# Kernel optimization log

Hardware: AMD Instinct MI355X
Metric: run time of the kernel (lower is better)

## Reference

```python
import jax, jax.numpy as jnp
import numpy as np

N = 50000          # num nodes
E = 800000         # num edges (before self loops)
IN_C = 128
HID = 256          # heads * head_dim
HEADS = 4
HEAD_DIM = HID // HEADS
OUT_C = 64
NEG_SLOPE = 0.2    # PyG GATConv default leaky_relu slope
BN_EPS = 1e-5


def _gat_conv(x, src, dst, W, att_src, att_dst, bias, concat):
    """PyG-style GATConv (with self loops already appended to src/dst).
    x: [N, in_c]; W: [in_c, H*C]; att_src/att_dst: [H, C]; bias: [H*C] or [C]."""
    H, C = att_src.shape
    h = (x @ W).reshape(-1, H, C)                               # [N, H, C]
    a_src = jnp.einsum('nhc,hc->nh', h, att_src)                # [N, H]
    a_dst = jnp.einsum('nhc,hc->nh', h, att_dst)                # [N, H]
    e = jax.nn.leaky_relu(a_src[src] + a_dst[dst], NEG_SLOPE)   # [Et, H]
    # segment softmax over destination nodes (numerically stable)
    m = jax.ops.segment_max(e, dst, num_segments=N)             # [N, H]
    m = jnp.where(jnp.isfinite(m), m, 0.0)
    ex = jnp.exp(e - m[dst])
    denom = jax.ops.segment_sum(ex, dst, num_segments=N)        # [N, H]
    alpha = ex / (denom[dst] + 1e-16)                           # [Et, H]
    msg = alpha[:, :, None] * h[src]                            # [Et, H, C]
    out = jax.ops.segment_sum(msg, dst, num_segments=N)         # [N, H, C]
    out = out.reshape(N, H * C) if concat else out.mean(axis=1)
    return out + bias


def _bn_eval(x, gamma, beta, mean, var):
    return (x - mean) * jax.lax.rsqrt(var + BN_EPS) * gamma + beta


def setup_inputs() -> dict:
    key = jax.random.key(0)
    ks = jax.random.split(key, 16)
    x = jax.random.normal(ks[0], (N, IN_C), dtype=jnp.float32)
    edge_index = jax.random.randint(ks[1], (2, E), 0, N, dtype=jnp.int64)

    def lin(k, fan_in, fan_out):
        s = (1.0 / np.sqrt(fan_in)).astype(np.float32)
        return jax.random.normal(k, (fan_in, fan_out), dtype=jnp.float32) * s

    def att(k, h, c):
        return jax.random.normal(k, (h, c), dtype=jnp.float32) * 0.1

    return {
        'x': x, 'edge_index': edge_index,
        'W0': lin(ks[2], IN_C, HID), 'as0': att(ks[3], HEADS, HEAD_DIM), 'ad0': att(ks[4], HEADS, HEAD_DIM), 'b0': jnp.zeros((HID,), jnp.float32),
        'bn0_g': jnp.ones((HID,), jnp.float32), 'bn0_b': jnp.zeros((HID,), jnp.float32), 'bn0_m': jnp.zeros((HID,), jnp.float32), 'bn0_v': jnp.ones((HID,), jnp.float32),
        'W1': lin(ks[5], HID, HID), 'as1': att(ks[6], HEADS, HEAD_DIM), 'ad1': att(ks[7], HEADS, HEAD_DIM), 'b1': jnp.zeros((HID,), jnp.float32),
        'bn1_g': jnp.ones((HID,), jnp.float32), 'bn1_b': jnp.zeros((HID,), jnp.float32), 'bn1_m': jnp.zeros((HID,), jnp.float32), 'bn1_v': jnp.ones((HID,), jnp.float32),
        'W2': lin(ks[8], HID, OUT_C), 'as2': att(ks[9], 1, OUT_C), 'ad2': att(ks[10], 1, OUT_C), 'b2': jnp.zeros((OUT_C,), jnp.float32),
    }


def reference(x, edge_index, W0, as0, ad0, b0, bn0_g, bn0_b, bn0_m, bn0_v,
              W1, as1, ad1, b1, bn1_g, bn1_b, bn1_m, bn1_v,
              W2, as2, ad2, b2):
    loop = jnp.arange(N, dtype=edge_index.dtype)
    src = jnp.concatenate([edge_index[0], loop])   # PyG add_self_loops=True
    dst = jnp.concatenate([edge_index[1], loop])

    h = _gat_conv(x, src, dst, W0, as0, ad0, b0, concat=True)
    h = jax.nn.elu(_bn_eval(h, bn0_g, bn0_b, bn0_m, bn0_v))   # dropout: eval -> identity
    h = _gat_conv(h, src, dst, W1, as1, ad1, b1, concat=True)
    h = jax.nn.elu(_bn_eval(h, bn1_g, bn1_b, bn1_m, bn1_v))
    out = _gat_conv(h, src, dst, W2, as2, ad2, b2, concat=False)  # heads=1, mean
    return out
```

## Files before the change

### kernel.cpp

```cpp
#include <hip/hip_runtime.h>

#define NN   50000
#define EE   800000
#define ET   850000
#define INC  128
#define HID  256
#define OUTC 64
#define NEG  0.2f
#define BNEPS 1e-5f

typedef __bf16 bf16x8 __attribute__((ext_vector_type(8)));
typedef float  f32x4  __attribute__((ext_vector_type(4)));

static __device__ __forceinline__ float b2f(unsigned short u) {
    return __uint_as_float(((unsigned)u) << 16);
}
static __device__ __forceinline__ float blo(unsigned u) {
    return __uint_as_float(u << 16);
}
static __device__ __forceinline__ float bhi(unsigned u) {
    return __uint_as_float(u & 0xFFFF0000u);
}
static __device__ __forceinline__ unsigned short f2b(float f) {
    unsigned u = __float_as_uint(f);
    unsigned r = u + 0x7FFFu + ((u >> 16) & 1u);
    return (unsigned short)(r >> 16);
}
static __device__ __forceinline__ float leaky(float x) {
    return x > 0.f ? x : NEG * x;
}
static __device__ __forceinline__ float ew(float e) {
    return __expf(fminf(e, 80.f));
}

__global__ void k_init(const int* __restrict__ ei, const unsigned* __restrict__ xw,
                       int* __restrict__ cnt, int* __restrict__ flagW, int* __restrict__ flagB,
                       int nbZ) {
    __shared__ int cs[4];
    int b = blockIdx.x, t = threadIdx.x;
    if (b < nbZ) {
        int i = b * 256 + t;
        if (i < NN) cnt[i] = 0;
    } else if (b == nbZ) {
        int c = 0;
        for (int k = 0; k < 16; k++) {
            int i = t + 256 * k;
            if (ei[2 * i + 1] != 0) c = 1;
        }
        for (int o = 1; o < 64; o <<= 1) c |= __shfl_xor(c, o);
        if ((t & 63) == 0) cs[t >> 6] = c;
        __syncthreads();
        if (t == 0) *flagW = cs[0] | cs[1] | cs[2] | cs[3];
    } else {
        int c = 0;
        for (int i = t; i < 4096; i += 256) {
            unsigned v = (xw[i] >> 8) & 0x7F;
            if (v >= 50 && v <= 67) c++;
        }
        for (int o = 1; o < 64; o <<= 1) c += __shfl_xor(c, o);
        if ((t & 63) == 0) cs[t >> 6] = c;
        __syncthreads();
        if (t == 0) *flagB = (cs[0] + cs[1] + cs[2] + cs[3] > 2048) ? 1 : 0;
    }
}

__global__ void k_prep(const void* as0, const void* ad0, const void* b0, const void* g0,
                       const void* be0, const void* m0, const void* v0,
                       const void* as1, const void* ad1, const void* b1, const void* g1,
                       const void* be1, const void* m1, const void* v1,
                       const void* as2, const void* ad2, const void* b2,
                       const void* W0, const void* W1, const void* W2,
                       unsigned short* __restrict__ WT0, unsigned short* __restrict__ WT1,
                       unsigned short* __restrict__ WT2,
                       const void* __restrict__ x, unsigned short* __restrict__ xb,
                       float* __restrict__ pp, const int* __restrict__ flagB) {
    int b = blockIdx.x, t = threadIdx.x;
    bool bf = (*flagB != 0);
    auto cv = [&](const void* s, int i) -> float {
        return bf ? b2f(((const unsigned short*)s)[i]) : ((const float*)s)[i];
    };
    if (b < 14) {
        float v;
        switch (b) {
            case 0:  v = cv(as0, t); break;
            case 1:  v = cv(ad0, t); break;
            case 2:  v = cv(b0, t);  break;
            case 3:  v = cv(g0, t);  break;
            case 4:  v = cv(be0, t); break;
            case 5:  v = cv(m0, t);  break;
            case 6:  v = cv(v0, t);  break;
            case 7:  v = cv(as1, t); break;
            case 8:  v = cv(ad1, t); break;
            case 9:  v = cv(b1, t);  break;
            case 10: v = cv(g1, t);  break;
            case 11: v = cv(be1, t); break;
            case 12: v = cv(m1, t);  break;
            default: v = cv(v1, t);  break;
        }
        pp[b * 256 + t] = v;
    } else if (b == 14) {
        if (t < 192) {
            int arr = t >> 6, j = t & 63;
            float v = (arr == 0) ? cv(as2, j) : (arr == 1) ? cv(ad2, j) : cv(b2, j);
            pp[14 * 256 + arr * 64 + j] = v;
        }
    } else if (b < 15 + 128) {
        int i = (b - 15) * 256 + t;
        int k = i >> 8, n = i & 255;
        WT0[n * INC + k] = bf ? ((const unsigned short*)W0)[i] : f2b(((const float*)W0)[i]);
    } else if (b < 15 + 128 + 256) {
        int i = (b - 143) * 256 + t;
        int k = i >> 8, n = i & 255;
        WT1[n * HID + k] = bf ? ((const unsigned short*)W1)[i] : f2b(((const float*)W1)[i]);
    } else if (b < 15 + 128 + 256 + 64) {
        int i = (b - 399) * 256 + t;
        int k = i >> 6, n = i & 63;
        WT2[n * HID + k] = bf ? ((const unsigned short*)W2)[i] : f2b(((const float*)W2)[i]);
    } else {
        if (bf) return;
        int i = (b - 463) * 256 + t;
        if (i < NN * INC)
            xb[i] = f2b(((const float*)x)[i]);
    }
}

__global__ void k_hist(const int* __restrict__ ei, const int* __restrict__ flagW,
                       int* __restrict__ cnt) {
    int i = blockIdx.x * 256 + threadIdx.x;
    if (i >= ET) return;
    bool w32 = (*flagW != 0);
    int d = (i < EE) ? (w32 ? ei[EE + i] : ei[2 * (EE + i)]) : (i - EE);
    atomicAdd(&cnt[d], 1);
}

static __device__ __forceinline__ int block_scan_incl(int v, int t, int* ws) {
    int lane = t & 63, w = t >> 6;
    int x = v;
    for (int o = 1; o < 64; o <<= 1) {
        int y = __shfl_up(x, o);
        if (lane >= o) x += y;
    }
    if (lane == 63) ws[w] = x;
    __syncthreads();
    if (t == 0) {
        int s = 0;
        for (int k = 0; k < 4; k++) { int tmp = ws[k]; ws[k] = s; s += tmp; }
    }
    __syncthreads();
    return x + ws[w];
}

__global__ void k_scan_a(const int* __restrict__ cnt, int* __restrict__ rowptr, int* __restrict__ bsum) {
    __shared__ int ws[4];
    int t = threadIdx.x, b = blockIdx.x;
    int i = b * 256 + t;
    int v = (i < NN) ? cnt[i] : 0;
    int incl = block_scan_incl(v, t, ws);
    if (i < NN) rowptr[i] = incl - v;
    if (t == 255) bsum[b] = incl;
}

__global__ void k_scan_b(int* __restrict__ bsum, int nb) {
    __shared__ int ws[4];
    int t = threadIdx.x;
    int v = (t < nb) ? bsum[t] : 0;
    int incl = block_scan_incl(v, t, ws);
    if (t < nb) bsum[t] = incl - v;
}

__global__ void k_scan_c(int* __restrict__ rowptr, const int* __restrict__ bsum, int* __restrict__ cursor) {
    int t = threadIdx.x, b = blockIdx.x;
    int i = b * 256 + t;
    if (i < NN) {
        int r = rowptr[i] + bsum[b];
        rowptr[i] = r;
        cursor[i] = r;
    }
    if (i == 0) rowptr[NN] = ET;
}

__global__ void k_scatter(const int* __restrict__ ei, const int* __restrict__ flagW,
                          int* __restrict__ cursor, int* __restrict__ esrc) {
    int i = blockIdx.x * 256 + threadIdx.x;
    if (i >= ET) return;
    bool w32 = (*flagW != 0);
    int s, d;
    if (i < EE) {
        if (w32) { s = ei[i];     d = ei[EE + i]; }
        else     { s = ei[2 * i]; d = ei[2 * (EE + i)]; }
    } else {
        s = d = i - EE;
    }
    int p = atomicAdd(&cursor[d], 1);
    esrc[p] = s;
}

template<int NC, int NH>
__global__ __launch_bounds__(256) void k_gemm(const unsigned short* __restrict__ Amain,
                                              const void* __restrict__ Aalt,
                                              const int* __restrict__ flagB,
                                              const unsigned short* __restrict__ WT,
                                              unsigned short* __restrict__ H,
                                              float* __restrict__ asrc, float* __restrict__ adst,
                                              const float* __restrict__ asv, const float* __restrict__ adv,
                                              int M, int K) {
    __shared__ __align__(16) unsigned short As[128 * 40];
    __shared__ __align__(16) unsigned short Bs[64 * 40];
    const unsigned short* A = (*flagB) ? (const unsigned short*)Aalt : Amain;
    int t = threadIdx.x;
    int bm = blockIdx.x, bn = blockIdx.y;
    int lane = t & 63, wave = t >> 6;
    int m16 = lane & 15, quad = lane >> 4;

    f32x4 acc[2][4];
    for (int a = 0; a < 2; a++) for (int b = 0; b < 4; b++) acc[a][b] = (f32x4){0.f, 0.f, 0.f, 0.f};

    int arow = t >> 1, ahalf = t & 1;
    int brow = t >> 2, bq = t & 3;
    long gArow = (long)bm * 128 + arow;

    for (int k0 = 0; k0 < K; k0 += 32) {
        uint4 av0 = {0u, 0u, 0u, 0u}, av1 = {0u, 0u, 0u, 0u};
        if (gArow < M) {
            const unsigned short* ap = A + gArow * (size_t)K + k0 + ahalf * 16;
            av0 = *(const uint4*)(ap);
            av1 = *(const uint4*)(ap + 8);
        }
        uint4 bv = *(const uint4*)(WT + ((size_t)bn * 64 + brow) * K + k0 + bq * 8);
        *(uint4*)&As[arow * 40 + ahalf * 16]     = av0;
        *(uint4*)&As[arow * 40 + ahalf * 16 + 8] = av1;
        *(uint4*)&Bs[brow * 40 + bq * 8]         = bv;
        __syncthreads();
        int wrow = wave * 32;
        bf16x8 af[2], bf[4];
        for (int mt = 0; mt < 2; mt++)
            af[mt] = *(const bf16x8*)&As[(wrow + mt * 16 + m16) * 40 + quad * 8];
        for (int nt = 0; nt < 4; nt++)
            bf[nt] = *(const bf16x8*)&Bs[(nt * 16 + m16) * 40 + quad * 8];
        for (int mt = 0; mt < 2; mt++)
            for (int nt = 0; nt < 4; nt++)
                acc[mt][nt] = __builtin_amdgcn_mfma_f32_16x16x32_bf16(af[mt], bf[nt], acc[mt][nt], 0, 0, 0);
        __syncthreads();
    }

    float asc[4], adc[4];
    for (int nt = 0; nt < 4; nt++) {
        int col = bn * 64 + nt * 16 + m16;
        asc[nt] = asv[col];
        adc[nt] = adv[col];
    }
    for (int mt = 0; mt < 2; mt++) {
        int gR0 = bm * 128 + wave * 32 + mt * 16 + quad * 4;
        for (int r = 0; r < 4; r++) {
            int gR = gR0 + r;
            float ps = 0.f, pd = 0.f;
            for (int nt = 0; nt < 4; nt++) {
                float v = acc[mt][nt][r];
                ps += v * asc[nt];
                pd += v * adc[nt];
            }
            for (int o = 1; o < 16; o <<= 1) { ps += __shfl_xor(ps, o); pd += __shfl_xor(pd, o); }
            if (m16 == 0 && gR < M) {
                asrc[(size_t)gR * NH + bn] = ps;
                adst[(size_t)gR * NH + bn] = pd;
            }
            if (gR < M) {
                for (int nt = 0; nt < 4; nt++) {
                    int gC = bn * 64 + nt * 16 + m16;
                    H[(size_t)gR * NC + gC] = f2b(acc[mt][nt][r]);
                }
            }
        }
    }
}

__global__ void k_agg4(const unsigned short* __restrict__ h,
                       const float* __restrict__ asrc, const float* __restrict__ adst,
                       const int* __restrict__ rowptr, const int* __restrict__ esrc,
                       const float* __restrict__ bias,
                       const float* __restrict__ bng, const float* __restrict__ bnb,
                       const float* __restrict__ bnm, const float* __restrict__ bnv,
                       unsigned short* __restrict__ act) {
    int t = threadIdx.x;
    int wave = t >> 6, lane = t & 63;
    int nodeA = blockIdx.x * 8 + wave * 2;
    if (nodeA >= NN) return;
    int nodeB = nodeA + 1;
    bool hasB = (nodeB < NN);

    int hd = lane >> 4, li = lane & 15;
    int wsel = lane & 48;
    const size_t lc = (size_t)lane * 4;

    int e0A = rowptr[nodeA];
    int e1A = rowptr[nodeA + 1];
    int degA = e1A - e0A;
    int e0B = 0, degB = 0;
    if (hasB) { e0B = e1A; degB = rowptr[nodeB + 1] - e1A; }
    float adhA = adst[(size_t)nodeA * 4 + hd];
    float adhB = hasB ? adst[(size_t)nodeB * 4 + hd] : 0.f;

    float waccA = 0.f, waccB = 0.f;
    float aA0 = 0.f, aA1 = 0.f, aA2 = 0.f, aA3 = 0.f;
    float aB0 = 0.f, aB1 = 0.f, aB2 = 0.f, aB3 = 0.f;

    int nA = min(16, degA), nB = min(16, degB);
    int sA = 0, sB = 0; float eA = 0.f, eB = 0.f;
    if (li < nA) { sA = esrc[e0A + li]; eA = asrc[(size_t)sA * 4 + hd]; }
    if (li < nB) { sB = esrc[e0B + li]; eB = asrc[(size_t)sB * 4 + hd]; }

    int degM = max(degA, degB);
    for (int c = 0; c < degM; c += 16) {
        float wA = (li < nA) ? ew(leaky(eA + adhA)) : 0.f;
        float wB = (li < nB) ? ew(leaky(eB + adhB)) : 0.f;
        waccA += wA; waccB += wB;
        int nA2 = min(16, degA - (c + 16));
        int nB2 = min(16, degB - (c + 16));
        int sA2 = 0, sB2 = 0; float eA2 = 0.f, eB2 = 0.f;
        if (li < nA2) { sA2 = esrc[e0A + c + 16 + li]; eA2 = asrc[(size_t)sA2 * 4 + hd]; }
        if (li < nB2) { sB2 = esrc[e0B + c + 16 + li]; eB2 = asrc[(size_t)sB2 * 4 + hd]; }
        #pragma unroll
        for (int g = 0; g < 4; g++) {
            int j = g * 4;
            bool doA = j < nA, doB = j < nB;
            int s0A = 0, s1A = 0, s2A = 0, s3A = 0;
            float w0A = 0.f, w1A = 0.f, w2A = 0.f, w3A = 0.f;
            ushort4 hA0 = {0, 0, 0, 0}, hA1 = {0, 0, 0, 0}, hA2 = {0, 0, 0, 0}, hA3 = {0, 0, 0, 0};
            int s0B = 0, s1B = 0, s2B = 0, s3B = 0;
            float w0B = 0.f, w1B = 0.f, w2B = 0.f, w3B = 0.f;
            ushort4 hB0 = {0, 0, 0, 0}, hB1 = {0, 0, 0, 0}, hB2 = {0, 0, 0, 0}, hB3 = {0, 0, 0, 0};
            if (doA) {
                s0A = __shfl(sA, j);     s1A = __shfl(sA, j + 1);
                s2A = __shfl(sA, j + 2); s3A = __shfl(sA, j + 3);
                w0A = __shfl(wA, wsel + j);     w1A = __shfl(wA, wsel + j + 1);
                w2A = __shfl(wA, wsel + j + 2); w3A = __shfl(wA, wsel + j + 3);
                hA0 = *(const ushort4*)(h + (size_t)s0A * HID + lc);
                hA1 = *(const ushort4*)(h + (size_t)s1A * HID + lc);
                hA2 = *(const ushort4*)(h + (size_t)s2A * HID + lc);
                hA3 = *(const ushort4*)(h + (size_t)s3A * HID + lc);
            }
            if (doB) {
                s0B = __shfl(sB, j);     s1B = __shfl(sB, j + 1);
                s2B = __shfl(sB, j + 2); s3B = __shfl(sB, j + 3);
                w0B = __shfl(wB, wsel + j);     w1B = __shfl(wB, wsel + j + 1);
                w2B = __shfl(wB, wsel + j + 2); w3B = __shfl(wB, wsel + j + 3);
                hB0 = *(const ushort4*)(h + (size_t)s0B * HID + lc);
                hB1 = *(const ushort4*)(h + (size_t)s1B * HID + lc);
                hB2 = *(const ushort4*)(h + (size_t)s2B * HID + lc);
                hB3 = *(const ushort4*)(h + (size_t)s3B * HID + lc);
            }
            if (doA) {
                aA0 += w0A * b2f(hA0.x) + w1A * b2f(hA1.x) + w2A * b2f(hA2.x) + w3A * b2f(hA3.x);
                aA1 += w0A * b2f(hA0.y) + w1A * b2f(hA1.y) + w2A * b2f(hA2.y) + w3A * b2f(hA3.y);
                aA2 += w0A * b2f(hA0.z) + w1A * b2f(hA1.z) + w2A * b2f(hA2.z) + w3A * b2f(hA3.z);
                aA3 += w0A * b2f(hA0.w) + w1A * b2f(hA1.w) + w2A * b2f(hA2.w) + w3A * b2f(hA3.w);
            }
            if (doB) {
                aB0 += w0B * b2f(hB0.x) + w1B * b2f(hB1.x) + w2B * b2f(hB2.x) + w3B * b2f(hB3.x);
                aB1 += w0B * b2f(hB0.y) + w1B * b2f(hB1.y) + w2B * b2f(hB2.y) + w3B * b2f(hB3.y);
                aB2 += w0B * b2f(hB0.z) + w1B * b2f(hB1.z) + w2B * b2f(hB2.z) + w3B * b2f(hB3.z);
                aB3 += w0B * b2f(hB0.w) + w1B * b2f(hB1.w) + w2B * b2f(hB2.w) + w3B * b2f(hB3.w);
            }
        }
        sA = sA2; eA = eA2; nA = nA2;
        sB = sB2; eB = eB2; nB = nB2;
    }
    waccA += __shfl_xor(waccA, 1); waccA += __shfl_xor(waccA, 2);
    waccA += __shfl_xor(waccA, 4); waccA += __shfl_xor(waccA, 8);
    waccB += __shfl_xor(waccB, 1); waccB += __shfl_xor(waccB, 2);
    waccB += __shfl_xor(waccB, 4); waccB += __shfl_xor(waccB, 8);
    float invA = 1.f / (waccA + 1e-16f);
    float invB = 1.f / (waccB + 1e-16f);

    int c0 = lane * 4;
    float4 bi = *(const float4*)(bias + c0);
    float4 bm_ = *(const float4*)(bnm + c0);
    float4 bv_ = *(const float4*)(bnv + c0);
    float4 bg_ = *(const float4*)(bng + c0);
    float4 bb_ = *(const float4*)(bnb + c0);
    float sc[4], sh[4];
    {
        const float* bvp = (const float*)&bv_;
        const float* bgp = (const float*)&bg_;
        const float* bmp = (const float*)&bm_;
        const float* bbp = (const float*)&bb_;
        const float* bip = (const float*)&bi;
        #pragma unroll
        for (int jj = 0; jj < 4; jj++) {
            float s_ = rsqrtf(bvp[jj] + BNEPS) * bgp[jj];
            sc[jj] = s_;
            sh[jj] = bbp[jj] + (bip[jj] - bmp[jj]) * s_;
        }
    }
    {
        float o[4] = {aA0 * invA, aA1 * invA, aA2 * invA, aA3 * invA};
        unsigned short res[4];
        #pragma unroll
        for (int jj = 0; jj < 4; jj++) {
            float val = o[jj] * sc[jj] + sh[jj];
            val = val > 0.f ? val : expm1f(val);
            res[jj] = f2b(val);
        }
        *(ushort4*)(act + (size_t)nodeA * HID + c0) = *(ushort4*)res;
    }
    if (hasB) {
        float o[4] = {aB0 * invB, aB1 * invB, aB2 * invB, aB3 * invB};
        unsigned short res[4];
        #pragma unroll
        for (int jj = 0; jj < 4; jj++) {
            float val = o[jj] * sc[jj] + sh[jj];
            val = val > 0.f ? val : expm1f(val);
            res[jj] = f2b(val);
        }
        *(ushort4*)(act + (size_t)nodeB * HID + c0) = *(ushort4*)res;
    }
}

__global__ __launch_bounds__(256, 4) void k_agg1(const unsigned short* __restrict__ h,
                       const float* __restrict__ asrc, const float* __restrict__ adst,
                       const int* __restrict__ rowptr, const int* __restrict__ esrc,
                       const float* __restrict__ bias,
                       void* __restrict__ outp, const int* __restrict__ flagB) {
    int t = threadIdx.x;
    int wave = t >> 6, lane = t & 63;
    int node = blockIdx.x * 4 + wave;
    if (node >= NN) return;
    int e0 = rowptr[node], deg = rowptr[node + 1] - e0;
    float ad = adst[node];
    int q = lane >> 4, laneQ = lane & 15;
    const size_t lc4 = (size_t)laneQ * 4;

    float den = 0.f;
    float a0 = 0.f, a1 = 0.f, a2 = 0.f, a3 = 0.f;

    int n = min(64, deg);
    int s = 0; float e = 0.f;
    if (lane < n) {
        s = esrc[e0 + lane];
        e = asrc[s];
    }

    for (int c = 0; c < deg; c += 64) {
        float w = (lane < n) ? ew(leaky(e + ad)) : 0.f;
        int n2 = min(64, deg - (c + 64));
        int sN = 0; float eN = 0.f;
        if (lane < n2) {
            sN = esrc[e0 + c + 64 + lane];
            eN = asrc[sN];
        }
        den += w;
        int ng = (n + 15) >> 4;
        #pragma unroll
        for (int g = 0; g < 4; g++) {
            if (g >= ng) break;
            int eb = g * 16 + q;
            int sA = __shfl(s, eb),      sB = __shfl(s, eb + 4);
            int sC = __shfl(s, eb + 8),  sD = __shfl(s, eb + 12);
            float wA = __shfl(w, eb),     wB = __shfl(w, eb + 4);
            float wC = __shfl(w, eb + 8), wD = __shfl(w, eb + 12);
            uint2 vA = *(const uint2*)(h + (size_t)sA * OUTC + lc4);
            uint2 vB = *(const uint2*)(h + (size_t)sB * OUTC + lc4);
            uint2 vC = *(const uint2*)(h + (size_t)sC * OUTC + lc4);
            uint2 vD = *(const uint2*)(h + (size_t)sD * OUTC + lc4);
            a0 += wA * blo(vA.x) + wB * blo(vB.x) + wC * blo(vC.x) + wD * blo(vD.x);
            a1 += wA * bhi(vA.x) + wB * bhi(vB.x) + wC * bhi(vC.x) + wD * bhi(vD.x);
            a2 += wA * blo(vA.y) + wB * blo(vB.y) + wC * blo(vC.y) + wD * blo(vD.y);
            a3 += wA * bhi(vA.y) + wB * bhi(vB.y) + wC * bhi(vC.y) + wD * bhi(vD.y);
        }
        s = sN; e = eN; n = n2;
    }
    for (int o = 1; o < 64; o <<= 1) den += __shfl_xor(den, o);
    a0 += __shfl_xor(a0, 16); a1 += __shfl_xor(a1, 16);
    a2 += __shfl_xor(a2, 16); a3 += __shfl_xor(a3, 16);
    a0 += __shfl_xor(a0, 32); a1 += __shfl_xor(a1, 32);
    a2 += __shfl_xor(a2, 32); a3 += __shfl_xor(a3, 32);
    float inv = 1.f / (den + 1e-16f);
    if (q == 0) {
        int c0 = laneQ * 4;
        float v0 = a0 * inv + bias[c0];
        float v1 = a1 * inv + bias[c0 + 1];
        float v2 = a2 * inv + bias[c0 + 2];
        float v3 = a3 * inv + bias[c0 + 3];
        if (*flagB) {
            unsigned r0 = (unsigned)f2b(v0) | ((unsigned)f2b(v1) << 16);
            unsigned r1 = (unsigned)f2b(v2) | ((unsigned)f2b(v3) << 16);
            uint2 rv = {r0, r1};
            *(uint2*)((unsigned short*)outp + (size_t)node * OUTC + c0) = rv;
        } else {
            float4 rv = {v0, v1, v2, v3};
            *(float4*)((float*)outp + (size_t)node * OUTC + c0) = rv;
        }
    }
}

extern "C" void kernel_launch(void* const* d_in, const int* in_sizes, int n_in,
                              void* d_out, int out_size, void* d_ws, size_t ws_size,
                              hipStream_t stream) {
    const void* x  = d_in[0];
    const int*  ei = (const int*)d_in[1];
    const void* W0 = d_in[2];
    const void* W1 = d_in[10];
    const void* W2 = d_in[18];

    char* ws = (char*)d_ws;
    size_t off = 0;
    auto alloc = [&](size_t n) { void* p = ws + off; off += (n + 255) & ~(size_t)255; return p; };

    unsigned short* xb  = (unsigned short*)alloc((size_t)NN * INC * 2);
    unsigned short* h   = (unsigned short*)alloc((size_t)NN * HID * 2);
    unsigned short* act = (unsigned short*)alloc((size_t)NN * HID * 2);
    unsigned short* WT0 = (unsigned short*)alloc((size_t)HID * INC * 2);
    unsigned short* WT1 = (unsigned short*)alloc((size_t)HID * HID * 2);
    unsigned short* WT2 = (unsigned short*)alloc((size_t)OUTC * HID * 2);
    float*          pp  = (float*)alloc((size_t)(14 * 256 + 3 * 64) * 4);
    float*  asrc   = (float*)alloc((size_t)NN * 4 * 4);
    float*  adst   = (float*)alloc((size_t)NN * 4 * 4);
    int*    cnt    = (int*)alloc((size_t)(NN + 2) * 4);
    int*    rowptr = (int*)alloc((size_t)(NN + 1) * 4);
    int*    cursor = (int*)alloc((size_t)NN * 4);
    int*    esrc   = (int*)alloc((size_t)ET * 4);
    int*    bsum   = (int*)alloc(256 * 4);
    int*    flagW  = cnt + NN;
    int*    flagB  = cnt + NN + 1;

    float* P0 = pp;
    float* P1 = pp + 7 * 256;
    float* P2 = pp + 14 * 256;

    const int nbN = (NN + 255) / 256;
    const int nbE = (ET + 255) / 256;
    const int nbA4 = (NN + 7) / 8;
    const int nbA1 = (NN + 3) / 4;
    const int nbPrep = 463 + (NN * INC + 255) / 256;
    dim3 gemmGrid0((NN + 127) / 128, HID / 64);
    dim3 gemmGrid2((NN + 127) / 128, 1);

    k_init<<<nbN + 2, 256, 0, stream>>>(ei, (const unsigned*)x, cnt, flagW, flagB, nbN);
    k_hist<<<nbE, 256, 0, stream>>>(ei, flagW, cnt);
    k_scan_a<<<nbN, 256, 0, stream>>>(cnt, rowptr, bsum);
    k_scan_b<<<1, 256, 0, stream>>>(bsum, nbN);
    k_scan_c<<<nbN, 256, 0, stream>>>(rowptr, bsum, cursor);
    k_scatter<<<nbE, 256, 0, stream>>>(ei, flagW, cursor, esrc);

    k_prep<<<nbPrep, 256, 0, stream>>>(d_in[3], d_in[4], d_in[5], d_in[6], d_in[7], d_in[8], d_in[9],
                                       d_in[11], d_in[12], d_in[13], d_in[14], d_in[15], d_in[16], d_in[17],
                                       d_in[19], d_in[20], d_in[21],
                                       W0, W1, W2, WT0, WT1, WT2, x, xb, pp, flagB);

    k_gemm<HID, 4><<<gemmGrid0, 256, 0, stream>>>(xb, x, flagB, WT0, h, asrc, adst,
                                                  P0 + 0, P0 + 256, NN, INC);
    k_agg4<<<nbA4, 256, 0, stream>>>(h, asrc, adst, rowptr, esrc,
                                     P0 + 512, P0 + 768, P0 + 1024, P0 + 1280, P0 + 1536, act);

    k_gemm<HID, 4><<<gemmGrid0, 256, 0, stream>>>(act, act, flagB, WT1, h, asrc, adst,
                                                  P1 + 0, P1 + 256, NN, HID);
    k_agg4<<<nbA4, 256, 0, stream>>>(h, asrc, adst, rowptr, esrc,
                                     P1 + 512, P1 + 768, P1 + 1024, P1 + 1280, P1 + 1536, act);

    k_gemm<OUTC, 1><<<gemmGrid2, 256, 0, stream>>>(act, act, flagB, WT2, h, asrc, adst,
                                                   P2 + 0, P2 + 64, NN, HID);
    k_agg1<<<nbA1, 256, 0, stream>>>(h, asrc, adst, rowptr, esrc, P2 + 128, d_out, flagB);
}
```

Measured before the change: 451.1 us.

## Load edge sources via scalar reads in aggregation and simplify agg1 layout

The aggregation kernels now make the row pointers wave-uniform with readfirstlane and load source indices directly from esrc (wave-uniform addresses, which can become scalar loads) instead of broadcasting them with shuffles. agg4 switches its bf16 gathers to uint2 with lo/hi unpacking. agg1 drops the quarter-wave multi-edge layout and its launch bounds in favour of one channel per lane, looping only over the valid edges. The count zeroing moves to hipMemsetAsync with a smaller flags kernel, and esrc is padded so reads past the end stay in bounds. The aim is to cut shuffle and VALU overhead. The risk is more load instructions and narrower per-lane gathers in agg1.

```diff
diff --git a/kernel.cpp b/kernel.cpp
--- a/kernel.cpp
+++ b/kernel.cpp
@@ -33,15 +33,11 @@
     return __expf(fminf(e, 80.f));
 }
 
-__global__ void k_init(const int* __restrict__ ei, const unsigned* __restrict__ xw,
-                       int* __restrict__ cnt, int* __restrict__ flagW, int* __restrict__ flagB,
-                       int nbZ) {
+__global__ void k_flags(const int* __restrict__ ei, const unsigned* __restrict__ xw,
+                        int* __restrict__ flagW, int* __restrict__ flagB) {
     __shared__ int cs[4];
     int b = blockIdx.x, t = threadIdx.x;
-    if (b < nbZ) {
-        int i = b * 256 + t;
-        if (i < NN) cnt[i] = 0;
-    } else if (b == nbZ) {
+    if (b == 0) {
         int c = 0;
         for (int k = 0; k < 16; k++) {
             int i = t + 256 * k;
@@ -292,11 +288,12 @@
     int wsel = lane & 48;
     const size_t lc = (size_t)lane * 4;
 
-    int e0A = rowptr[nodeA];
-    int e1A = rowptr[nodeA + 1];
+    int e0A = __builtin_amdgcn_readfirstlane(rowptr[nodeA]);
+    int e1A = __builtin_amdgcn_readfirstlane(rowptr[nodeA + 1]);
     int degA = e1A - e0A;
-    int e0B = 0, degB = 0;
-    if (hasB) { e0B = e1A; degB = rowptr[nodeB + 1] - e1A; }
+    int e0B = e1A, degB = 0;
+    if (hasB) degB = __builtin_amdgcn_readfirstlane(rowptr[nodeB + 1]) - e1A;
+
     float adhA = adst[(size_t)nodeA * 4 + hd];
     float adhB = hasB ? adst[(size_t)nodeB * 4 + hd] : 0.f;
 
@@ -305,9 +302,9 @@
     float aB0 = 0.f, aB1 = 0.f, aB2 = 0.f, aB3 = 0.f;
 
     int nA = min(16, degA), nB = min(16, degB);
-    int sA = 0, sB = 0; float eA = 0.f, eB = 0.f;
-    if (li < nA) { sA = esrc[e0A + li]; eA = asrc[(size_t)sA * 4 + hd]; }
-    if (li < nB) { sB = esrc[e0B + li]; eB = asrc[(size_t)sB * 4 + hd]; }
+    float eA = 0.f, eB = 0.f;
+    if (li < nA) { int s = esrc[e0A + li]; eA = asrc[(size_t)s * 4 + hd]; }
+    if (li < nB) { int s = esrc[e0B + li]; eB = asrc[(size_t)s * 4 + hd]; }
 
     int degM = max(degA, degB);
     for (int c = 0; c < degM; c += 16) {
@@ -316,54 +313,52 @@
         waccA += wA; waccB += wB;
         int nA2 = min(16, degA - (c + 16));
         int nB2 = min(16, degB - (c + 16));
-        int sA2 = 0, sB2 = 0; float eA2 = 0.f, eB2 = 0.f;
-        if (li < nA2) { sA2 = esrc[e0A + c + 16 + li]; eA2 = asrc[(size_t)sA2 * 4 + hd]; }
-        if (li < nB2) { sB2 = esrc[e0B + c + 16 + li]; eB2 = asrc[(size_t)sB2 * 4 + hd]; }
+        float eA2 = 0.f, eB2 = 0.f;
+        if (li < nA2) { int s = esrc[e0A + c + 16 + li]; eA2 = asrc[(size_t)s * 4 + hd]; }
+        if (li < nB2) { int s = esrc[e0B + c + 16 + li]; eB2 = asrc[(size_t)s * 4 + hd]; }
         #pragma unroll
         for (int g = 0; g < 4; g++) {
             int j = g * 4;
             bool doA = j < nA, doB = j < nB;
-            int s0A = 0, s1A = 0, s2A = 0, s3A = 0;
             float w0A = 0.f, w1A = 0.f, w2A = 0.f, w3A = 0.f;
-            ushort4 hA0 = {0, 0, 0, 0}, hA1 = {0, 0, 0, 0}, hA2 = {0, 0, 0, 0}, hA3 = {0, 0, 0, 0};
-            int s0B = 0, s1B = 0, s2B = 0, s3B = 0;
             float w0B = 0.f, w1B = 0.f, w2B = 0.f, w3B = 0.f;
-            ushort4 hB0 = {0, 0, 0, 0}, hB1 = {0, 0, 0, 0}, hB2 = {0, 0, 0, 0}, hB3 = {0, 0, 0, 0};
+            uint2 hA0 = {0, 0}, hA1 = {0, 0}, hA2 = {0, 0}, hA3 = {0, 0};
+            uint2 hB0 = {0, 0}, hB1 = {0, 0}, hB2 = {0, 0}, hB3 = {0, 0};
             if (doA) {
-                s0A = __shfl(sA, j);     s1A = __shfl(sA, j + 1);
-                s2A = __shfl(sA, j + 2); s3A = __shfl(sA, j + 3);
+                int s0 = esrc[e0A + c + j];     int s1 = esrc[e0A + c + j + 1];
+                int s2 = esrc[e0A + c + j + 2]; int s3 = esrc[e0A + c + j + 3];
                 w0A = __shfl(wA, wsel + j);     w1A = __shfl(wA, wsel + j + 1);
                 w2A = __shfl(wA, wsel + j + 2); w3A = __shfl(wA, wsel + j + 3);
-                hA0 = *(const ushort4*)(h + (size_t)s0A * HID + lc);
-                hA1 = *(const ushort4*)(h + (size_t)s1A * HID + lc);
-                hA2 = *(const ushort4*)(h + (size_t)s2A * HID + lc);
-                hA3 = *(const ushort4*)(h + (size_t)s3A * HID + lc);
+                hA0 = *(const uint2*)(h + (size_t)s0 * HID + lc);
+                hA1 = *(const uint2*)(h + (size_t)s1 * HID + lc);
+                hA2 = *(const uint2*)(h + (size_t)s2 * HID + lc);
+                hA3 = *(const uint2*)(h + (size_t)s3 * HID + lc);
             }
             if (doB) {
-                s0B = __shfl(sB, j);     s1B = __shfl(sB, j + 1);
-                s2B = __shfl(sB, j + 2); s3B = __shfl(sB, j + 3);
+                int s0 = esrc[e0B + c + j];     int s1 = esrc[e0B + c + j + 1];
+                int s2 = esrc[e0B + c + j + 2]; int s3 = esrc[e0B + c + j + 3];
                 w0B = __shfl(wB, wsel + j);     w1B = __shfl(wB, wsel + j + 1);
                 w2B = __shfl(wB, wsel + j + 2); w3B = __shfl(wB, wsel + j + 3);
-                hB0 = *(const ushort4*)(h + (size_t)s0B * HID + lc);
-                hB1 = *(const ushort4*)(h + (size_t)s1B * HID + lc);
-                hB2 = *(const ushort4*)(h + (size_t)s2B * HID + lc);
-                hB3 = *(const ushort4*)(h + (size_t)s3B * HID + lc);
+                hB0 = *(const uint2*)(h + (size_t)s0 * HID + lc);
+                hB1 = *(const uint2*)(h + (size_t)s1 * HID + lc);
+                hB2 = *(const uint2*)(h + (size_t)s2 * HID + lc);
+                hB3 = *(const uint2*)(h + (size_t)s3 * HID + lc);
             }
             if (doA) {
-                aA0 += w0A * b2f(hA0.x) + w1A * b2f(hA1.x) + w2A * b2f(hA2.x) + w3A * b2f(hA3.x);
-                aA1 += w0A * b2f(hA0.y) + w1A * b2f(hA1.y) + w2A * b2f(hA2.y) + w3A * b2f(hA3.y);
-                aA2 += w0A * b2f(hA0.z) + w1A * b2f(hA1.z) + w2A * b2f(hA2.z) + w3A * b2f(hA3.z);
-                aA3 += w0A * b2f(hA0.w) + w1A * b2f(hA1.w) + w2A * b2f(hA2.w) + w3A * b2f(hA3.w);
+                aA0 += w0A * blo(hA0.x) + w1A * blo(hA1.x) + w2A * blo(hA2.x) + w3A * blo(hA3.x);
+                aA1 += w0A * bhi(hA0.x) + w1A * bhi(hA1.x) + w2A * bhi(hA2.x) + w3A * bhi(hA3.x);
+                aA2 += w0A * blo(hA0.y) + w1A * blo(hA1.y) + w2A * blo(hA2.y) + w3A * blo(hA3.y);
+                aA3 += w0A * bhi(hA0.y) + w1A * bhi(hA1.y) + w2A * bhi(hA2.y) + w3A * bhi(hA3.y);
             }
             if (doB) {
-                aB0 += w0B * b2f(hB0.x) + w1B * b2f(hB1.x) + w2B * b2f(hB2.x) + w3B * b2f(hB3.x);
-                aB1 += w0B * b2f(hB0.y) + w1B * b2f(hB1.y) + w2B * b2f(hB2.y) + w3B * b2f(hB3.y);
-                aB2 += w0B * b2f(hB0.z) + w1B * b2f(hB1.z) + w2B * b2f(hB2.z) + w3B * b2f(hB3.z);
-                aB3 += w0B * b2f(hB0.w) + w1B * b2f(hB1.w) + w2B * b2f(hB2.w) + w3B * b2f(hB3.w);
-            }
-        }
-        sA = sA2; eA = eA2; nA = nA2;
-        sB = sB2; eB = eB2; nB = nB2;
+                aB0 += w0B * blo(hB0.x) + w1B * blo(hB1.x) + w2B * blo(hB2.x) + w3B * blo(hB3.x);
+                aB1 += w0B * bhi(hB0.x) + w1B * bhi(hB1.x) + w2B * bhi(hB2.x) + w3B * bhi(hB3.x);
+                aB2 += w0B * blo(hB0.y) + w1B * blo(hB1.y) + w2B * blo(hB2.y) + w3B * blo(hB3.y);
+                aB3 += w0B * bhi(hB0.y) + w1B * bhi(hB1.y) + w2B * bhi(hB2.y) + w3B * bhi(hB3.y);
+            }
+        }
+        eA = eA2; nA = nA2;
+        eB = eB2; nB = nB2;
     }
     waccA += __shfl_xor(waccA, 1); waccA += __shfl_xor(waccA, 2);
     waccA += __shfl_xor(waccA, 4); waccA += __shfl_xor(waccA, 8);
@@ -416,7 +411,7 @@
     }
 }
 
-__global__ __launch_bounds__(256, 4) void k_agg1(const unsigned short* __restrict__ h,
+__global__ void k_agg1(const unsigned short* __restrict__ h,
                        const float* __restrict__ asrc, const float* __restrict__ adst,
                        const int* __restrict__ rowptr, const int* __restrict__ esrc,
                        const float* __restrict__ bias,
@@ -425,72 +420,40 @@
     int wave = t >> 6, lane = t & 63;
     int node = blockIdx.x * 4 + wave;
     if (node >= NN) return;
-    int e0 = rowptr[node], deg = rowptr[node + 1] - e0;
+    int e0  = __builtin_amdgcn_readfirstlane(rowptr[node]);
+    int e1  = __builtin_amdgcn_readfirstlane(rowptr[node + 1]);
+    int deg = e1 - e0;
     float ad = adst[node];
-    int q = lane >> 4, laneQ = lane & 15;
-    const size_t lc4 = (size_t)laneQ * 4;
-
-    float den = 0.f;
-    float a0 = 0.f, a1 = 0.f, a2 = 0.f, a3 = 0.f;
+
+    float den = 0.f, acc = 0.f;
 
     int n = min(64, deg);
-    int s = 0; float e = 0.f;
-    if (lane < n) {
-        s = esrc[e0 + lane];
-        e = asrc[s];
-    }
+    float e = 0.f;
+    if (lane < n) { int s = esrc[e0 + lane]; e = asrc[s]; }
 
     for (int c = 0; c < deg; c += 64) {
         float w = (lane < n) ? ew(leaky(e + ad)) : 0.f;
         int n2 = min(64, deg - (c + 64));
-        int sN = 0; float eN = 0.f;
-        if (lane < n2) {
-            sN = esrc[e0 + c + 64 + lane];
-            eN = asrc[sN];
-        }
+        float eN = 0.f;
+        if (lane < n2) { int s = esrc[e0 + c + 64 + lane]; eN = asrc[s]; }
         den += w;
-        int ng = (n + 15) >> 4;
-        #pragma unroll
-        for (int g = 0; g < 4; g++) {
-            if (g >= ng) break;
-            int eb = g * 16 + q;
-            int sA = __shfl(s, eb),      sB = __shfl(s, eb + 4);
-            int sC = __shfl(s, eb + 8),  sD = __shfl(s, eb + 12);
-            float wA = __shfl(w, eb),     wB = __shfl(w, eb + 4);
-            float wC = __shfl(w, eb + 8), wD = __shfl(w, eb + 12);
-            uint2 vA = *(const uint2*)(h + (size_t)sA * OUTC + lc4);
-            uint2 vB = *(const uint2*)(h + (size_t)sB * OUTC + lc4);
-            uint2 vC = *(const uint2*)(h + (size_t)sC * OUTC + lc4);
-            uint2 vD = *(const uint2*)(h + (size_t)sD * OUTC + lc4);
-            a0 += wA * blo(vA.x) + wB * blo(vB.x) + wC * blo(vC.x) + wD * blo(vD.x);
-            a1 += wA * bhi(vA.x) + wB * bhi(vB.x) + wC * bhi(vC.x) + wD * bhi(vD.x);
-            a2 += wA * blo(vA.y) + wB * blo(vB.y) + wC * blo(vC.y) + wD * blo(vD.y);
-            a3 += wA * bhi(vA.y) + wB * bhi(vB.y) + wC * bhi(vC.y) + wD * bhi(vD.y);
-        }
-        s = sN; e = eN; n = n2;
+        for (int j = 0; j < n; j += 4) {
+            int s0 = esrc[e0 + c + j];     int s1 = esrc[e0 + c + j + 1];
+            int s2 = esrc[e0 + c + j + 2]; int s3 = esrc[e0 + c + j + 3];
+            float w0 = __shfl(w, j),     w1 = __shfl(w, j + 1);
+            float w2 = __shfl(w, j + 2), w3 = __shfl(w, j + 3);
+            float h0 = b2f(h[(size_t)s0 * OUTC + lane]);
+            float h1 = b2f(h[(size_t)s1 * OUTC + lane]);
+            float h2 = b2f(h[(size_t)s2 * OUTC + lane]);
+            float h3 = b2f(h[(size_t)s3 * OUTC + lane]);
+            acc += w0 * h0 + w1 * h1 + w2 * h2 + w3 * h3;
+        }
+        e = eN; n = n2;
     }
     for (int o = 1; o < 64; o <<= 1) den += __shfl_xor(den, o);
-    a0 += __shfl_xor(a0, 16); a1 += __shfl_xor(a1, 16);
-    a2 += __shfl_xor(a2, 16); a3 += __shfl_xor(a3, 16);
-    a0 += __shfl_xor(a0, 32); a1 += __shfl_xor(a1, 32);
-    a2 += __shfl_xor(a2, 32); a3 += __shfl_xor(a3, 32);
-    float inv = 1.f / (den + 1e-16f);
-    if (q == 0) {
-        int c0 = laneQ * 4;
-        float v0 = a0 * inv + bias[c0];
-        float v1 = a1 * inv + bias[c0 + 1];
-        float v2 = a2 * inv + bias[c0 + 2];
-        float v3 = a3 * inv + bias[c0 + 3];
-        if (*flagB) {
-            unsigned r0 = (unsigned)f2b(v0) | ((unsigned)f2b(v1) << 16);
-            unsigned r1 = (unsigned)f2b(v2) | ((unsigned)f2b(v3) << 16);
-            uint2 rv = {r0, r1};
-            *(uint2*)((unsigned short*)outp + (size_t)node * OUTC + c0) = rv;
-        } else {
-            float4 rv = {v0, v1, v2, v3};
-            *(float4*)((float*)outp + (size_t)node * OUTC + c0) = rv;
-        }
-    }
+    float val = acc / (den + 1e-16f) + bias[lane];
+    if (*flagB) ((unsigned short*)outp)[(size_t)node * OUTC + lane] = f2b(val);
+    else        ((float*)outp)[(size_t)node * OUTC + lane] = val;
 }
 
 extern "C" void kernel_launch(void* const* d_in, const int* in_sizes, int n_in,
@@ -518,7 +481,7 @@
     int*    cnt    = (int*)alloc((size_t)(NN + 2) * 4);
     int*    rowptr = (int*)alloc((size_t)(NN + 1) * 4);
     int*    cursor = (int*)alloc((size_t)NN * 4);
-    int*    esrc   = (int*)alloc((size_t)ET * 4);
+    int*    esrc   = (int*)alloc((size_t)(ET + 64) * 4);
     int*    bsum   = (int*)alloc(256 * 4);
     int*    flagW  = cnt + NN;
     int*    flagB  = cnt + NN + 1;
@@ -535,7 +498,8 @@
     dim3 gemmGrid0((NN + 127) / 128, HID / 64);
     dim3 gemmGrid2((NN + 127) / 128, 1);
 
-    k_init<<<nbN + 2, 256, 0, stream>>>(ei, (const unsigned*)x, cnt, flagW, flagB, nbN);
+    hipMemsetAsync(cnt, 0, (size_t)(NN + 2) * 4, stream);
+    k_flags<<<2, 256, 0, stream>>>(ei, (const unsigned*)x, flagW, flagB);
     k_hist<<<nbE, 256, 0, stream>>>(ei, flagW, cnt);
     k_scan_a<<<nbN, 256, 0, stream>>>(cnt, rowptr, bsum);
     k_scan_b<<<1, 256, 0, stream>>>(bsum, nbN);
```

After: 447.8 us. About the same (-0.7%).
